# Performance work log

Hardware: AMD Instinct MI355X
Metric: run time of the kernel (lower is better)

The kernel has to match this reference:

```python
import jax, jax.numpy as jnp
import numpy as np

NUM_GROUPS = 32
NUM_HEADS = 8
EPS = 1e-5


def setup_inputs() -> dict:
    key = jax.random.key(0)
    ks = jax.random.split(key, 4)
    b, c, h, w = 16, 512, 32, 32
    x = jax.random.normal(ks[0], (b, c, h, w), dtype=jnp.float32)
    norm_w = jnp.ones((c,), dtype=jnp.float32)
    norm_b = jnp.zeros((c,), dtype=jnp.float32)
    qkv_w = jax.random.normal(ks[1], (3 * c, c), dtype=jnp.float32) * (1.0 / np.sqrt(c))
    qkv_b = jnp.zeros((3 * c,), dtype=jnp.float32)
    proj_w = jax.random.normal(ks[2], (c, c), dtype=jnp.float32) * (1.0 / np.sqrt(c))
    proj_b = jnp.zeros((c,), dtype=jnp.float32)
    return {"x": x, "norm_w": norm_w, "norm_b": norm_b,
            "qkv_w": qkv_w, "qkv_b": qkv_b, "proj_w": proj_w, "proj_b": proj_b}


def group_norm(x, weight, bias):
    b, c, h, w = x.shape
    xg = x.reshape(b, NUM_GROUPS, c // NUM_GROUPS, h * w)
    mean = xg.mean(axis=(2, 3), keepdims=True)
    var = xg.var(axis=(2, 3), keepdims=True)
    xn = (xg - mean) * jax.lax.rsqrt(var + EPS)
    xn = xn.reshape(b, c, h, w)
    return xn * weight[None, :, None, None] + bias[None, :, None, None]


def reference(x, norm_w, norm_b, qkv_w, qkv_b, proj_w, proj_b):
    b, c, h, w = x.shape
    n = h * w
    head = NUM_HEADS
    ch = c // head

    x_norm = group_norm(x, norm_w, norm_b)
    # 1x1 conv == channel matmul: [b,3c,n]
    xf = x_norm.reshape(b, c, n)
    qkv = jnp.einsum('oc,bcn->bon', qkv_w, xf) + qkv_b[None, :, None]
    q, k, v = jnp.split(qkv, 3, axis=1)  # each [b,c,n]
    q = q.reshape(b, head, ch, n) * (ch ** -0.5)
    k = k.reshape(b, head, ch, n)
    v = v.reshape(b, head, ch, n)

    attn = jnp.einsum('bhcn,bhcm->bhnm', q, k)
    attn = jax.nn.softmax(attn, axis=-1)
    out = jnp.einsum('bhnm,bhcm->bhcn', attn, v)  # [b,head,ch,n]
    out = out.reshape(b, c, n)
    out = jnp.einsum('oc,bcn->bon', proj_w, out) + proj_b[None, :, None]
    return x + out.reshape(b, c, h, w)
```

## Files before the change

kernel.cpp:

```cpp
#include <hip/hip_runtime.h>

typedef short short8 __attribute__((ext_vector_type(8)));
typedef float f32x4 __attribute__((ext_vector_type(4)));

#define B_   16
#define C_   512
#define N_   1024
#define NH_  8
#define CH_  64
#define G_   32
#define CPG_ 16

__device__ inline float b2f(unsigned int u) {
    union { unsigned int i; float f; } v; v.i = u << 16; return v.f;
}
__device__ inline unsigned short f2b(float f) {
    union { float f; unsigned int i; } v; v.f = f;
    unsigned int r = v.i + 0x7fffu + ((v.i >> 16) & 1u);
    return (unsigned short)(r >> 16);
}
__device__ inline unsigned int pack2(float a, float b) {
    return (unsigned int)f2b(a) | ((unsigned int)f2b(b) << 16);
}
__device__ inline unsigned int asu(float f) {
    union { float f; unsigned int i; } v; v.f = f; return v.i;
}
__device__ inline unsigned int packtr(float a, float b) {
    return __builtin_amdgcn_perm(asu(b), asu(a), 0x07060302u);
}
__device__ inline void gload16(const void* g, void* l) {
    __builtin_amdgcn_global_load_lds(
        (const __attribute__((address_space(1))) void*)g,
        (__attribute__((address_space(3))) void*)l, 16, 0, 0);
}

__global__ __launch_bounds__(256) void gnconv_kernel(const float* __restrict__ x,
                                                     const float* __restrict__ nw,
                                                     const float* __restrict__ nb,
                                                     unsigned short* __restrict__ xnT,
                                                     const float* __restrict__ qkvw,
                                                     const float* __restrict__ projw,
                                                     unsigned short* __restrict__ wq,
                                                     unsigned short* __restrict__ wp)
{
    __shared__ float red[8];
    __shared__ unsigned short T[64 * 17];
    int t = threadIdx.x;

    if (blockIdx.x >= 512) {
        const int NQ = 3 * C_ * C_;
        int idx = (((int)blockIdx.x - 512) * 256 + t) * 8;
        const float* src; unsigned short* dst; int j;
        if (idx < NQ) { src = qkvw;  dst = wq; j = idx; }
        else          { src = projw; dst = wp; j = idx - NQ; }
        float4 u0 = *(const float4*)(src + j);
        float4 u1 = *(const float4*)(src + j + 4);
        uint4 p;
        p.x = pack2(u0.x, u0.y); p.y = pack2(u0.z, u0.w);
        p.z = pack2(u1.x, u1.y); p.w = pack2(u1.z, u1.w);
        *(uint4*)(dst + j) = p;
        return;
    }

    int b = blockIdx.x >> 5, g = blockIdx.x & 31;
    const float* base = x + ((size_t)(b * C_ + g * CPG_)) * N_;

    float s = 0.f, ss = 0.f;
    for (int it = 0; it < 16; ++it) {
        int idx = (it * 256 + t) * 4;
        float4 u = *(const float4*)(base + idx);
        s  += u.x + u.y + u.z + u.w;
        ss += u.x * u.x + u.y * u.y + u.z * u.z + u.w * u.w;
    }
#pragma unroll
    for (int off = 1; off < 64; off <<= 1) {
        s  += __shfl_xor(s, off);
        ss += __shfl_xor(ss, off);
    }
    int wv = t >> 6;
    if ((t & 63) == 0) { red[wv * 2] = s; red[wv * 2 + 1] = ss; }
    __syncthreads();
    s  = red[0] + red[2] + red[4] + red[6];
    ss = red[1] + red[3] + red[5] + red[7];
    float mean = s * (1.f / 16384.f);
    float var  = ss * (1.f / 16384.f) - mean * mean;
    float rstd = rsqrtf(var + 1e-5f);

    int cl = t >> 4, nn4 = (t & 15) * 4;
    float sc = nw[g * CPG_ + cl] * rstd;
    float sh = nb[g * CPG_ + cl] - mean * sc;
    int nlB = t >> 2, c4 = (t & 3) * 4;

    for (int ch = 0; ch < 16; ++ch) {
        int n0 = ch * 64;
        float4 u = *(const float4*)(base + (size_t)cl * N_ + n0 + nn4);
        T[(nn4 + 0) * 17 + cl] = f2b(u.x * sc + sh);
        T[(nn4 + 1) * 17 + cl] = f2b(u.y * sc + sh);
        T[(nn4 + 2) * 17 + cl] = f2b(u.z * sc + sh);
        T[(nn4 + 3) * 17 + cl] = f2b(u.w * sc + sh);
        __syncthreads();
        ushort4 o;
        o.x = T[nlB * 17 + c4 + 0];
        o.y = T[nlB * 17 + c4 + 1];
        o.z = T[nlB * 17 + c4 + 2];
        o.w = T[nlB * 17 + c4 + 3];
        *(ushort4*)(xnT + ((size_t)(b * N_ + n0 + nlB)) * C_ + g * CPG_ + c4) = o;
        __syncthreads();
    }
}

__global__ __launch_bounds__(256) void qkv_kernel(const unsigned short* __restrict__ w,
                                                  const float* __restrict__ bias,
                                                  const unsigned short* __restrict__ xnT,
                                                  unsigned short* __restrict__ qT,
                                                  unsigned short* __restrict__ kT,
                                                  unsigned short* __restrict__ vv)
{
    __shared__ unsigned short Als[128 * 32], Bls[128 * 32];
    int t = threadIdx.x;
    int n0 = blockIdx.x * 128, m0 = blockIdx.y * 128, b = blockIdx.z;
    int lane = t & 63, wv = t >> 6;
    int l = lane & 15, qd = lane >> 4;
    int wm = (wv >> 1) * 64, wn = (wv & 1) * 64;
    f32x4 acc[4][4] = {};
    const unsigned short* Bbase = xnT + ((size_t)(b * N_ + n0)) * C_;

    int lr = lane >> 2, bpos = lane & 3;
    int r0 = wv * 32 + lr, r1 = r0 + 16;
    int c0 = (bpos ^ ((r0 >> 1) & 3)) * 8;
    int c1 = (bpos ^ ((r1 >> 1) & 3)) * 8;
    const unsigned short* gA0 = w + (size_t)(m0 + r0) * C_ + c0;
    const unsigned short* gA1 = w + (size_t)(m0 + r1) * C_ + c1;
    const unsigned short* gB0 = Bbase + (size_t)r0 * C_ + c0;
    const unsigned short* gB1 = Bbase + (size_t)r1 * C_ + c1;
    unsigned short* lA0 = &Als[(wv * 32) * 32];
    unsigned short* lA1 = &Als[(wv * 32 + 16) * 32];
    unsigned short* lB0 = &Bls[(wv * 32) * 32];
    unsigned short* lB1 = &Bls[(wv * 32 + 16) * 32];

    int aoff[4], boff[4];
#pragma unroll
    for (int i = 0; i < 4; ++i) {
        int ra = wm + i * 16 + l;
        aoff[i] = ra * 32 + ((qd ^ ((ra >> 1) & 3)) * 8);
        int rb = wn + i * 16 + l;
        boff[i] = rb * 32 + ((qd ^ ((rb >> 1) & 3)) * 8);
    }

    for (int kk = 0; kk < 16; ++kk) {
        int ko = kk * 32;
        gload16(gA0 + ko, lA0); gload16(gA1 + ko, lA1);
        gload16(gB0 + ko, lB0); gload16(gB1 + ko, lB1);
        __builtin_amdgcn_s_waitcnt(0);
        __syncthreads();
        short8 aF[4], bF[4];
#pragma unroll
        for (int i = 0; i < 4; ++i) {
            aF[i] = *(const short8*)&Als[aoff[i]];
            bF[i] = *(const short8*)&Bls[boff[i]];
        }
#pragma unroll
        for (int mt = 0; mt < 4; ++mt)
#pragma unroll
            for (int nt = 0; nt < 4; ++nt)
                acc[mt][nt] = __builtin_amdgcn_mfma_f32_16x16x32_bf16(aF[mt], bF[nt], acc[mt][nt], 0, 0, 0);
        __syncthreads();
    }

    int o_base = m0 + wm;
    int sec = o_base >> 9;
    int oc = o_base & 511;
    int h = oc >> 6;
    float bv[4][4];
#pragma unroll
    for (int mt = 0; mt < 4; ++mt)
#pragma unroll
        for (int r = 0; r < 4; ++r)
            bv[mt][r] = bias[o_base + mt * 16 + qd * 4 + r];

    if (sec < 2) {
        unsigned short* dst = (sec == 0) ? qT : kT;
        float scl = (sec == 0) ? (0.125f * 1.44269504f) : 1.0f;
#pragma unroll
        for (int mt = 0; mt < 4; ++mt)
#pragma unroll
            for (int nt = 0; nt < 4; ++nt) {
                int n = n0 + wn + nt * 16 + l;
                ushort4 o;
                o.x = f2b((acc[mt][nt][0] + bv[mt][0]) * scl);
                o.y = f2b((acc[mt][nt][1] + bv[mt][1]) * scl);
                o.z = f2b((acc[mt][nt][2] + bv[mt][2]) * scl);
                o.w = f2b((acc[mt][nt][3] + bv[mt][3]) * scl);
                *(ushort4*)(dst + ((size_t)(b * NH_ + h) * N_ + n) * CH_ + mt * 16 + qd * 4) = o;
            }
    } else {
#pragma unroll
        for (int mt = 0; mt < 4; ++mt)
#pragma unroll
            for (int nt = 0; nt < 4; ++nt) {
                int n = n0 + wn + nt * 16 + l;
#pragma unroll
                for (int r = 0; r < 4; ++r) {
                    int ch = mt * 16 + qd * 4 + r;
                    vv[((size_t)(b * NH_ + h) * CH_ + ch) * N_ + n] = f2b(acc[mt][nt][r] + bv[mt][r]);
                }
            }
    }
}

__global__ __launch_bounds__(256, 4) void attn_kernel(const unsigned short* __restrict__ qT,
                                                      const unsigned short* __restrict__ kT,
                                                      const unsigned short* __restrict__ vv,
                                                      unsigned short* __restrict__ at)
{
    __shared__ unsigned short Ks[2][4096];
    __shared__ unsigned short Vs[2][4096];

    int t = threadIdx.x, lane = t & 63, wv = t >> 6;
    int l = lane & 15, qd = lane >> 4;
    int blk = blockIdx.x;
    int ibk = blk >> 7;
    int bh  = blk & 127;
    int h = bh & 7, b = bh >> 3;
    int i0 = ibk * 128 + wv * 32;
    const size_t hoff = (size_t)bh * (size_t)N_ * CH_;
    const unsigned short* qbase = qT + hoff;
    const unsigned short* kbase = kT + hoff;
    const unsigned short* vbase = vv + hoff;

    int plok;
    {
        unsigned int ta = (unsigned int)lane, tb = 64u + (unsigned int)lane;
        asm volatile("v_permlane32_swap_b32 %0, %1" : "+v"(ta), "+v"(tb));
        asm volatile("v_permlane16_swap_b32 %0, %1" : "+v"(ta), "+v"(tb));
        unsigned int e1 = (unsigned int)((lane >> 4) * 32 + (lane & 15));
        plok = __all(ta == e1) && __all(tb == e1 + 16u);
    }

    short8 qF[2][2];
#pragma unroll
    for (int it = 0; it < 2; ++it)
#pragma unroll
        for (int ks = 0; ks < 2; ++ks)
            qF[it][ks] = *(const short8*)(qbase + (size_t)(i0 + it * 16 + l) * CH_ + ks * 32 + qd * 8);

    int srow = t >> 2, sc16 = (t & 3) * 16;
    int sw = srow & 7, bb = (t & 3) * 2;
    int d0 = srow * 64 + ((bb ^ sw) * 8);
    int d1 = srow * 64 + (((bb + 1) ^ sw) * 8);
    const unsigned short* kSrc = kbase + (size_t)srow * CH_ + sc16;
    const unsigned short* vSrc = vbase + (size_t)srow * N_ + sc16;

    f32x4 Oa[4][2] = {};
    float lsum[2] = {0.f, 0.f};
    int la0 = (qd & 1) * 32 + l;
    int la1 = la0 + 16;
    int swl = l & 7;

    uint4 ku0, ku1, vu0, vu1;
    {
        const uint4* kp = (const uint4*)(kSrc);
        ku0 = kp[0]; ku1 = kp[1];
        const uint4* vp2 = (const uint4*)(vSrc);
        vu0 = vp2[0]; vu1 = vp2[1];
        *(uint4*)&Ks[0][d0] = ku0; *(uint4*)&Ks[0][d1] = ku1;
        *(uint4*)&Vs[0][d0] = vu0; *(uint4*)&Vs[0][d1] = vu1;
        kp  = (const uint4*)(kSrc + 4096);
        ku0 = kp[0]; ku1 = kp[1];
        vp2 = (const uint4*)(vSrc + 64);
        vu0 = vp2[0]; vu1 = vp2[1];
    }

    for (int tile = 0; tile < 16; ++tile) {
        __syncthreads();
        if (tile < 15) {
            unsigned short* Kw = Ks[(tile + 1) & 1];
            unsigned short* Vw = Vs[(tile + 1) & 1];
            *(uint4*)&Kw[d0] = ku0; *(uint4*)&Kw[d1] = ku1;
            *(uint4*)&Vw[d0] = vu0; *(uint4*)&Vw[d1] = vu1;
            if (tile < 14) {
                const uint4* kp = (const uint4*)(kSrc + (size_t)(tile + 2) * 4096);
                ku0 = kp[0]; ku1 = kp[1];
                const uint4* vp2 = (const uint4*)(vSrc + (size_t)(tile + 2) * 64);
                vu0 = vp2[0]; vu1 = vp2[1];
            }
        }
        const unsigned short* Kb = Ks[tile & 1];
        const unsigned short* Vb = Vs[tile & 1];
#pragma unroll
        for (int jb = 0; jb < 2; ++jb) {
            short8 kA[2][2];
#pragma unroll
            for (int jt = 0; jt < 2; ++jt)
#pragma unroll
                for (int ks = 0; ks < 2; ++ks)
                    kA[jt][ks] = *(const short8*)&Kb[(jb * 32 + jt * 16 + l) * 64 + (((ks * 4 + qd) ^ swl) * 8)];
            f32x4 Sa[2][2] = {};
#pragma unroll
            for (int jt = 0; jt < 2; ++jt)
#pragma unroll
                for (int it = 0; it < 2; ++it)
#pragma unroll
                    for (int ks = 0; ks < 2; ++ks)
                        Sa[jt][it] = __builtin_amdgcn_mfma_f32_16x16x32_bf16(kA[jt][ks], qF[it][ks], Sa[jt][it], 0, 0, 0);
            unsigned int pk[2][2][2];
#pragma unroll
            for (int jt = 0; jt < 2; ++jt)
#pragma unroll
                for (int it = 0; it < 2; ++it) {
                    float p0 = __builtin_amdgcn_exp2f(Sa[jt][it][0]);
                    float p1 = __builtin_amdgcn_exp2f(Sa[jt][it][1]);
                    float p2 = __builtin_amdgcn_exp2f(Sa[jt][it][2]);
                    float p3 = __builtin_amdgcn_exp2f(Sa[jt][it][3]);
                    lsum[it] += (p0 + p1) + (p2 + p3);
                    pk[jt][it][0] = packtr(p0, p1);
                    pk[jt][it][1] = packtr(p2, p3);
                }
            short8 bP[2];
            if (plok) {
#pragma unroll
                for (int it = 0; it < 2; ++it) {
                    union { short8 s; unsigned int u[4]; } fb;
                    unsigned int a0 = pk[0][it][0], c0 = pk[1][it][0];
                    asm volatile("v_permlane32_swap_b32 %0, %1" : "+v"(a0), "+v"(c0));
                    asm volatile("v_permlane16_swap_b32 %0, %1" : "+v"(a0), "+v"(c0));
                    unsigned int a1 = pk[0][it][1], c1 = pk[1][it][1];
                    asm volatile("v_permlane32_swap_b32 %0, %1" : "+v"(a1), "+v"(c1));
                    asm volatile("v_permlane16_swap_b32 %0, %1" : "+v"(a1), "+v"(c1));
                    fb.u[0] = a0; fb.u[1] = a1; fb.u[2] = c0; fb.u[3] = c1;
                    bP[it] = fb.s;
                }
            } else {
#pragma unroll
                for (int it = 0; it < 2; ++it) {
                    union { short8 s; unsigned int u[4]; } fb;
                    unsigned int a0 = (unsigned int)__shfl((int)pk[0][it][0], la0);
                    unsigned int b0 = (unsigned int)__shfl((int)pk[1][it][0], la0);
                    fb.u[0] = (qd < 2) ? a0 : b0;
                    unsigned int a1 = (unsigned int)__shfl((int)pk[0][it][1], la0);
                    unsigned int b1 = (unsigned int)__shfl((int)pk[1][it][1], la0);
                    fb.u[1] = (qd < 2) ? a1 : b1;
                    unsigned int a2 = (unsigned int)__shfl((int)pk[0][it][0], la1);
                    unsigned int b2 = (unsigned int)__shfl((int)pk[1][it][0], la1);
                    fb.u[2] = (qd < 2) ? a2 : b2;
                    unsigned int a3 = (unsigned int)__shfl((int)pk[0][it][1], la1);
                    unsigned int b3 = (unsigned int)__shfl((int)pk[1][it][1], la1);
                    fb.u[3] = (qd < 2) ? a3 : b3;
                    bP[it] = fb.s;
                }
            }
            short8 vA[4];
#pragma unroll
            for (int cht = 0; cht < 4; ++cht)
                vA[cht] = *(const short8*)&Vb[(cht * 16 + l) * 64 + (((jb * 4 + qd) ^ swl) * 8)];
#pragma unroll
            for (int cht = 0; cht < 4; ++cht)
#pragma unroll
                for (int it = 0; it < 2; ++it)
                    Oa[cht][it] = __builtin_amdgcn_mfma_f32_16x16x32_bf16(vA[cht], bP[it], Oa[cht][it], 0, 0, 0);
        }
    }

#pragma unroll
    for (int it = 0; it < 2; ++it) {
        float lt = lsum[it];
        lt += __shfl_xor(lt, 16);
        lt += __shfl_xor(lt, 32);
        float inv = 1.0f / lt;
        int i = i0 + it * 16 + l;
        unsigned short* dst = at + ((size_t)(b * N_ + i)) * C_ + h * CH_;
#pragma unroll
        for (int cht = 0; cht < 4; ++cht) {
            ushort4 o;
            o.x = f2b(Oa[cht][it][0] * inv);
            o.y = f2b(Oa[cht][it][1] * inv);
            o.z = f2b(Oa[cht][it][2] * inv);
            o.w = f2b(Oa[cht][it][3] * inv);
            *(ushort4*)(dst + cht * 16 + qd * 4) = o;
        }
    }
}

__global__ __launch_bounds__(256) void proj_kernel(const unsigned short* __restrict__ w,
                                                   const float* __restrict__ bias,
                                                   const unsigned short* __restrict__ at,
                                                   const float* __restrict__ x,
                                                   float* __restrict__ out)
{
    __shared__ unsigned short Als[128 * 32], Bls[128 * 32];
    int t = threadIdx.x;
    int n0 = blockIdx.x * 128, m0 = blockIdx.y * 128, b = blockIdx.z;
    int lane = t & 63, wv = t >> 6;
    int l = lane & 15, qd = lane >> 4;
    int wm = (wv >> 1) * 64, wn = (wv & 1) * 64;
    f32x4 acc[4][4] = {};
    const unsigned short* Bbase = at + ((size_t)(b * N_ + n0)) * C_;

    int lr = lane >> 2, bpos = lane & 3;
    int r0 = wv * 32 + lr, r1 = r0 + 16;
    int c0 = (bpos ^ ((r0 >> 1) & 3)) * 8;
    int c1 = (bpos ^ ((r1 >> 1) & 3)) * 8;
    const unsigned short* gA0 = w + (size_t)(m0 + r0) * C_ + c0;
    const unsigned short* gA1 = w + (size_t)(m0 + r1) * C_ + c1;
    const unsigned short* gB0 = Bbase + (size_t)r0 * C_ + c0;
    const unsigned short* gB1 = Bbase + (size_t)r1 * C_ + c1;
    unsigned short* lA0 = &Als[(wv * 32) * 32];
    unsigned short* lA1 = &Als[(wv * 32 + 16) * 32];
    unsigned short* lB0 = &Bls[(wv * 32) * 32];
    unsigned short* lB1 = &Bls[(wv * 32 + 16) * 32];

    int aoff[4], boff[4];
#pragma unroll
    for (int i = 0; i < 4; ++i) {
        int ra = wm + i * 16 + l;
        aoff[i] = ra * 32 + ((qd ^ ((ra >> 1) & 3)) * 8);
        int rb = wn + i * 16 + l;
        boff[i] = rb * 32 + ((qd ^ ((rb >> 1) & 3)) * 8);
    }

    for (int kk = 0; kk < 16; ++kk) {
        int ko = kk * 32;
        gload16(gA0 + ko, lA0); gload16(gA1 + ko, lA1);
        gload16(gB0 + ko, lB0); gload16(gB1 + ko, lB1);
        __builtin_amdgcn_s_waitcnt(0);
        __syncthreads();
        short8 aF[4], bF[4];
#pragma unroll
        for (int i = 0; i < 4; ++i) {
            aF[i] = *(const short8*)&Als[aoff[i]];
            bF[i] = *(const short8*)&Bls[boff[i]];
        }
#pragma unroll
        for (int mt = 0; mt < 4; ++mt)
#pragma unroll
            for (int nt = 0; nt < 4; ++nt)
                acc[mt][nt] = __builtin_amdgcn_mfma_f32_16x16x32_bf16(aF[mt], bF[nt], acc[mt][nt], 0, 0, 0);
        __syncthreads();
    }

    float bv[4][4];
#pragma unroll
    for (int mt = 0; mt < 4; ++mt)
#pragma unroll
        for (int r = 0; r < 4; ++r)
            bv[mt][r] = bias[m0 + wm + mt * 16 + qd * 4 + r];

#pragma unroll
    for (int mt = 0; mt < 4; ++mt)
#pragma unroll
        for (int nt = 0; nt < 4; ++nt) {
            int n = n0 + wn + nt * 16 + l;
#pragma unroll
            for (int r = 0; r < 4; ++r) {
                int o = m0 + wm + mt * 16 + qd * 4 + r;
                size_t idx = ((size_t)b * C_ + o) * N_ + n;
                out[idx] = acc[mt][nt][r] + bv[mt][r] + x[idx];
            }
        }
}

extern "C" void kernel_launch(void* const* d_in, const int* in_sizes, int n_in,
                              void* d_out, int out_size, void* d_ws, size_t ws_size,
                              hipStream_t stream) {
    const float* x     = (const float*)d_in[0];
    const float* nw    = (const float*)d_in[1];
    const float* nb    = (const float*)d_in[2];
    const float* qkvw  = (const float*)d_in[3];
    const float* qkvb  = (const float*)d_in[4];
    const float* projw = (const float*)d_in[5];
    const float* projb = (const float*)d_in[6];
    float* out = (float*)d_out;
    char* ws = (char*)d_ws;
    const size_t SZ = (size_t)B_ * N_ * C_ * 2;
    unsigned short* xnT = (unsigned short*)(ws);
    unsigned short* qTp = (unsigned short*)(ws + SZ);
    unsigned short* kTp = (unsigned short*)(ws + 2 * SZ);
    unsigned short* vp  = (unsigned short*)(ws + 3 * SZ);
    unsigned short* atp = (unsigned short*)(ws);
    unsigned short* wq  = (unsigned short*)(ws + 4 * SZ);
    unsigned short* wp  = (unsigned short*)(ws + 4 * SZ + (size_t)3 * C_ * C_ * 2);

    hipLaunchKernelGGL(gnconv_kernel, dim3(1024), dim3(256), 0, stream, x, nw, nb, xnT, qkvw, projw, wq, wp);
    hipLaunchKernelGGL(qkv_kernel,    dim3(8, 12, B_), dim3(256), 0, stream, wq, qkvb, xnT, qTp, kTp, vp);
    hipLaunchKernelGGL(attn_kernel,   dim3(1024), dim3(256), 0, stream, qTp, kTp, vp, atp);
    hipLaunchKernelGGL(proj_kernel,   dim3(8, 4, B_), dim3(256), 0, stream, wp, projb, atp, x, out);
}
```

Before: 219.1 us.

## Widen GEMM K-tile to 64, drop LDS transpose in groupnorm, batch attention tile

The QKV and projection GEMMs now stage a 64-wide K slice per iteration with an 8-way XOR swizzle, which halves the loop trips and barrier pairs. The cost is double the LDS per block. The groupnorm kernel no longer transposes through shared memory with two barriers per chunk. Each thread instead loads all 16 channels for two positions and writes 32-byte bf16 rows directly. The attention inner loop is restructured to issue both key sub-blocks' loads, QK MFMAs, exps and P permutes together before the PV MFMAs, giving more ILP at the cost of more registers.

```diff
diff --git a/kernel.cpp b/kernel.cpp
--- a/kernel.cpp
+++ b/kernel.cpp
@@ -44,7 +44,6 @@
                                                      unsigned short* __restrict__ wp)
 {
     __shared__ float red[8];
-    __shared__ unsigned short T[64 * 17];
     int t = threadIdx.x;
 
     if (blockIdx.x >= 512) {
@@ -86,26 +85,39 @@
     float var  = ss * (1.f / 16384.f) - mean * mean;
     float rstd = rsqrtf(var + 1e-5f);
 
-    int cl = t >> 4, nn4 = (t & 15) * 4;
-    float sc = nw[g * CPG_ + cl] * rstd;
-    float sh = nb[g * CPG_ + cl] - mean * sc;
-    int nlB = t >> 2, c4 = (t & 3) * 4;
-
+    float sc[16], sh[16];
+#pragma unroll
     for (int ch = 0; ch < 16; ++ch) {
-        int n0 = ch * 64;
-        float4 u = *(const float4*)(base + (size_t)cl * N_ + n0 + nn4);
-        T[(nn4 + 0) * 17 + cl] = f2b(u.x * sc + sh);
-        T[(nn4 + 1) * 17 + cl] = f2b(u.y * sc + sh);
-        T[(nn4 + 2) * 17 + cl] = f2b(u.z * sc + sh);
-        T[(nn4 + 3) * 17 + cl] = f2b(u.w * sc + sh);
-        __syncthreads();
-        ushort4 o;
-        o.x = T[nlB * 17 + c4 + 0];
-        o.y = T[nlB * 17 + c4 + 1];
-        o.z = T[nlB * 17 + c4 + 2];
-        o.w = T[nlB * 17 + c4 + 3];
-        *(ushort4*)(xnT + ((size_t)(b * N_ + n0 + nlB)) * C_ + g * CPG_ + c4) = o;
-        __syncthreads();
+        float wv_ = nw[g * CPG_ + ch];
+        float bv_ = nb[g * CPG_ + ch];
+        sc[ch] = wv_ * rstd;
+        sh[ch] = bv_ - mean * sc[ch];
+    }
+
+#pragma unroll
+    for (int nbi = 0; nbi < 2; ++nbi) {
+        int n = nbi * 512 + t * 2;
+        float2 v[16];
+#pragma unroll
+        for (int ch = 0; ch < 16; ++ch)
+            v[ch] = *(const float2*)(base + (size_t)ch * N_ + n);
+#pragma unroll
+        for (int col = 0; col < 2; ++col) {
+            float f[16];
+#pragma unroll
+            for (int ch = 0; ch < 16; ++ch) {
+                float xv = col ? v[ch].y : v[ch].x;
+                f[ch] = xv * sc[ch] + sh[ch];
+            }
+            uint4 o0, o1;
+            o0.x = pack2(f[0], f[1]);  o0.y = pack2(f[2], f[3]);
+            o0.z = pack2(f[4], f[5]);  o0.w = pack2(f[6], f[7]);
+            o1.x = pack2(f[8], f[9]);  o1.y = pack2(f[10], f[11]);
+            o1.z = pack2(f[12], f[13]); o1.w = pack2(f[14], f[15]);
+            unsigned short* dst = xnT + ((size_t)(b * N_ + n + col)) * C_ + g * CPG_;
+            *(uint4*)dst = o0;
+            *(uint4*)(dst + 8) = o1;
+        }
     }
 }
 
@@ -116,7 +128,7 @@
                                                   unsigned short* __restrict__ kT,
                                                   unsigned short* __restrict__ vv)
 {
-    __shared__ unsigned short Als[128 * 32], Bls[128 * 32];
+    __shared__ unsigned short Als[128 * 64], Bls[128 * 64];
     int t = threadIdx.x;
     int n0 = blockIdx.x * 128, m0 = blockIdx.y * 128, b = blockIdx.z;
     int lane = t & 63, wv = t >> 6;
@@ -125,45 +137,43 @@
     f32x4 acc[4][4] = {};
     const unsigned short* Bbase = xnT + ((size_t)(b * N_ + n0)) * C_;
 
-    int lr = lane >> 2, bpos = lane & 3;
-    int r0 = wv * 32 + lr, r1 = r0 + 16;
-    int c0 = (bpos ^ ((r0 >> 1) & 3)) * 8;
-    int c1 = (bpos ^ ((r1 >> 1) & 3)) * 8;
-    const unsigned short* gA0 = w + (size_t)(m0 + r0) * C_ + c0;
-    const unsigned short* gA1 = w + (size_t)(m0 + r1) * C_ + c1;
-    const unsigned short* gB0 = Bbase + (size_t)r0 * C_ + c0;
-    const unsigned short* gB1 = Bbase + (size_t)r1 * C_ + c1;
-    unsigned short* lA0 = &Als[(wv * 32) * 32];
-    unsigned short* lA1 = &Als[(wv * 32 + 16) * 32];
-    unsigned short* lB0 = &Bls[(wv * 32) * 32];
-    unsigned short* lB1 = &Bls[(wv * 32 + 16) * 32];
-
-    int aoff[4], boff[4];
-#pragma unroll
-    for (int i = 0; i < 4; ++i) {
-        int ra = wm + i * 16 + l;
-        aoff[i] = ra * 32 + ((qd ^ ((ra >> 1) & 3)) * 8);
-        int rb = wn + i * 16 + l;
-        boff[i] = rb * 32 + ((qd ^ ((rb >> 1) & 3)) * 8);
-    }
-
-    for (int kk = 0; kk < 16; ++kk) {
-        int ko = kk * 32;
-        gload16(gA0 + ko, lA0); gload16(gA1 + ko, lA1);
-        gload16(gB0 + ko, lB0); gload16(gB1 + ko, lB1);
+    int grow = lane >> 3, gcol = ((lane & 7) ^ grow) * 8;
+    const unsigned short* pA[4]; const unsigned short* pB[4];
+    unsigned short* lA[4]; unsigned short* lB[4];
+#pragma unroll
+    for (int g = 0; g < 4; ++g) {
+        int r = wv * 32 + g * 8 + grow;
+        pA[g] = w + (size_t)(m0 + r) * C_ + gcol;
+        pB[g] = Bbase + (size_t)r * C_ + gcol;
+        lA[g] = &Als[(wv * 32 + g * 8) * 64];
+        lB[g] = &Bls[(wv * 32 + g * 8) * 64];
+    }
+
+    for (int kk = 0; kk < 8; ++kk) {
+        int ko = kk * 64;
+#pragma unroll
+        for (int g = 0; g < 4; ++g) {
+            gload16(pA[g] + ko, lA[g]);
+            gload16(pB[g] + ko, lB[g]);
+        }
         __builtin_amdgcn_s_waitcnt(0);
         __syncthreads();
-        short8 aF[4], bF[4];
-#pragma unroll
-        for (int i = 0; i < 4; ++i) {
-            aF[i] = *(const short8*)&Als[aoff[i]];
-            bF[i] = *(const short8*)&Bls[boff[i]];
-        }
-#pragma unroll
-        for (int mt = 0; mt < 4; ++mt)
-#pragma unroll
-            for (int nt = 0; nt < 4; ++nt)
-                acc[mt][nt] = __builtin_amdgcn_mfma_f32_16x16x32_bf16(aF[mt], bF[nt], acc[mt][nt], 0, 0, 0);
+#pragma unroll
+        for (int ks = 0; ks < 2; ++ks) {
+            short8 aF[4], bF[4];
+#pragma unroll
+            for (int i = 0; i < 4; ++i) {
+                int ra = wm + i * 16 + l;
+                aF[i] = *(const short8*)&Als[ra * 64 + (((ks * 4 + qd) ^ (l & 7)) * 8)];
+                int rb = wn + i * 16 + l;
+                bF[i] = *(const short8*)&Bls[rb * 64 + (((ks * 4 + qd) ^ (l & 7)) * 8)];
+            }
+#pragma unroll
+            for (int mt = 0; mt < 4; ++mt)
+#pragma unroll
+                for (int nt = 0; nt < 4; ++nt)
+                    acc[mt][nt] = __builtin_amdgcn_mfma_f32_16x16x32_bf16(aF[mt], bF[nt], acc[mt][nt], 0, 0, 0);
+        }
         __syncthreads();
     }
 
@@ -287,68 +297,85 @@
         }
         const unsigned short* Kb = Ks[tile & 1];
         const unsigned short* Vb = Vs[tile & 1];
-#pragma unroll
-        for (int jb = 0; jb < 2; ++jb) {
-            short8 kA[2][2];
+
+        short8 kA[2][2][2];
+#pragma unroll
+        for (int jb = 0; jb < 2; ++jb)
 #pragma unroll
             for (int jt = 0; jt < 2; ++jt)
 #pragma unroll
                 for (int ks = 0; ks < 2; ++ks)
-                    kA[jt][ks] = *(const short8*)&Kb[(jb * 32 + jt * 16 + l) * 64 + (((ks * 4 + qd) ^ swl) * 8)];
-            f32x4 Sa[2][2] = {};
+                    kA[jb][jt][ks] = *(const short8*)&Kb[(jb * 32 + jt * 16 + l) * 64 + (((ks * 4 + qd) ^ swl) * 8)];
+        f32x4 Sa[2][2][2] = {};
+#pragma unroll
+        for (int jb = 0; jb < 2; ++jb)
 #pragma unroll
             for (int jt = 0; jt < 2; ++jt)
 #pragma unroll
                 for (int it = 0; it < 2; ++it)
 #pragma unroll
                     for (int ks = 0; ks < 2; ++ks)
-                        Sa[jt][it] = __builtin_amdgcn_mfma_f32_16x16x32_bf16(kA[jt][ks], qF[it][ks], Sa[jt][it], 0, 0, 0);
-            unsigned int pk[2][2][2];
+                        Sa[jb][jt][it] = __builtin_amdgcn_mfma_f32_16x16x32_bf16(kA[jb][jt][ks], qF[it][ks], Sa[jb][jt][it], 0, 0, 0);
+
+        unsigned int pk[2][2][2][2];
+        float ls0 = 0.f, ls1 = 0.f;
+#pragma unroll
+        for (int jb = 0; jb < 2; ++jb)
 #pragma unroll
             for (int jt = 0; jt < 2; ++jt)
 #pragma unroll
                 for (int it = 0; it < 2; ++it) {
-                    float p0 = __builtin_amdgcn_exp2f(Sa[jt][it][0]);
-                    float p1 = __builtin_amdgcn_exp2f(Sa[jt][it][1]);
-                    float p2 = __builtin_amdgcn_exp2f(Sa[jt][it][2]);
-                    float p3 = __builtin_amdgcn_exp2f(Sa[jt][it][3]);
-                    lsum[it] += (p0 + p1) + (p2 + p3);
-                    pk[jt][it][0] = packtr(p0, p1);
-                    pk[jt][it][1] = packtr(p2, p3);
+                    float p0 = __builtin_amdgcn_exp2f(Sa[jb][jt][it][0]);
+                    float p1 = __builtin_amdgcn_exp2f(Sa[jb][jt][it][1]);
+                    float p2 = __builtin_amdgcn_exp2f(Sa[jb][jt][it][2]);
+                    float p3 = __builtin_amdgcn_exp2f(Sa[jb][jt][it][3]);
+                    float q01 = (p0 + p1) + (p2 + p3);
+                    if (it == 0) ls0 += q01; else ls1 += q01;
+                    pk[jb][jt][it][0] = packtr(p0, p1);
+                    pk[jb][jt][it][1] = packtr(p2, p3);
                 }
-            short8 bP[2];
-            if (plok) {
+        lsum[0] += ls0; lsum[1] += ls1;
+
+        short8 bP[2][2];
+        if (plok) {
+#pragma unroll
+            for (int jb = 0; jb < 2; ++jb)
 #pragma unroll
                 for (int it = 0; it < 2; ++it) {
                     union { short8 s; unsigned int u[4]; } fb;
-                    unsigned int a0 = pk[0][it][0], c0 = pk[1][it][0];
+                    unsigned int a0 = pk[jb][0][it][0], c0 = pk[jb][1][it][0];
                     asm volatile("v_permlane32_swap_b32 %0, %1" : "+v"(a0), "+v"(c0));
                     asm volatile("v_permlane16_swap_b32 %0, %1" : "+v"(a0), "+v"(c0));
-                    unsigned int a1 = pk[0][it][1], c1 = pk[1][it][1];
+                    unsigned int a1 = pk[jb][0][it][1], c1 = pk[jb][1][it][1];
                     asm volatile("v_permlane32_swap_b32 %0, %1" : "+v"(a1), "+v"(c1));
                     asm volatile("v_permlane16_swap_b32 %0, %1" : "+v"(a1), "+v"(c1));
                     fb.u[0] = a0; fb.u[1] = a1; fb.u[2] = c0; fb.u[3] = c1;
-                    bP[it] = fb.s;
+                    bP[jb][it] = fb.s;
                 }
-            } else {
+        } else {
+#pragma unroll
+            for (int jb = 0; jb < 2; ++jb)
 #pragma unroll
                 for (int it = 0; it < 2; ++it) {
                     union { short8 s; unsigned int u[4]; } fb;
-                    unsigned int a0 = (unsigned int)__shfl((int)pk[0][it][0], la0);
-                    unsigned int b0 = (unsigned int)__shfl((int)pk[1][it][0], la0);
+                    unsigned int a0 = (unsigned int)__shfl((int)pk[jb][0][it][0], la0);
+                    unsigned int b0 = (unsigned int)__shfl((int)pk[jb][1][it][0], la0);
                     fb.u[0] = (qd < 2) ? a0 : b0;
-                    unsigned int a1 = (unsigned int)__shfl((int)pk[0][it][1], la0);
-                    unsigned int b1 = (unsigned int)__shfl((int)pk[1][it][1], la0);
+                    unsigned int a1 = (unsigned int)__shfl((int)pk[jb][0][it][1], la0);
+                    unsigned int b1 = (unsigned int)__shfl((int)pk[jb][1][it][1], la0);
                     fb.u[1] = (qd < 2) ? a1 : b1;
-                    unsigned int a2 = (unsigned int)__shfl((int)pk[0][it][0], la1);
-                    unsigned int b2 = (unsigned int)__shfl((int)pk[1][it][0], la1);
+                    unsigned int a2 = (unsigned int)__shfl((int)pk[jb][0][it][0], la1);
+                    unsigned int b2 = (unsigned int)__shfl((int)pk[jb][1][it][0], la1);
                     fb.u[2] = (qd < 2) ? a2 : b2;
-                    unsigned int a3 = (unsigned int)__shfl((int)pk[0][it][1], la1);
-                    unsigned int b3 = (unsigned int)__shfl((int)pk[1][it][1], la1);
+                    unsigned int a3 = (unsigned int)__shfl((int)pk[jb][0][it][1], la1);
+                    unsigned int b3 = (unsigned int)__shfl((int)pk[jb][1][it][1], la1);
                     fb.u[3] = (qd < 2) ? a3 : b3;
-                    bP[it] = fb.s;
+                    bP[jb][it] = fb.s;
                 }
-            }
+        }
+
+#pragma unroll
+        for (int jb = 0; jb < 2; ++jb) {
             short8 vA[4];
 #pragma unroll
             for (int cht = 0; cht < 4; ++cht)
@@ -357,7 +384,7 @@
             for (int cht = 0; cht < 4; ++cht)
 #pragma unroll
                 for (int it = 0; it < 2; ++it)
-                    Oa[cht][it] = __builtin_amdgcn_mfma_f32_16x16x32_bf16(vA[cht], bP[it], Oa[cht][it], 0, 0, 0);
+                    Oa[cht][it] = __builtin_amdgcn_mfma_f32_16x16x32_bf16(vA[cht], bP[jb][it], Oa[cht][it], 0, 0, 0);
         }
     }
 
@@ -387,7 +414,7 @@
                                                    const float* __restrict__ x,
                                                    float* __restrict__ out)
 {
-    __shared__ unsigned short Als[128 * 32], Bls[128 * 32];
+    __shared__ unsigned short Als[128 * 64], Bls[128 * 64];
     int t = threadIdx.x;
     int n0 = blockIdx.x * 128, m0 = blockIdx.y * 128, b = blockIdx.z;
     int lane = t & 63, wv = t >> 6;
@@ -396,45 +423,43 @@
     f32x4 acc[4][4] = {};
     const unsigned short* Bbase = at + ((size_t)(b * N_ + n0)) * C_;
 
-    int lr = lane >> 2, bpos = lane & 3;
-    int r0 = wv * 32 + lr, r1 = r0 + 16;
-    int c0 = (bpos ^ ((r0 >> 1) & 3)) * 8;
-    int c1 = (bpos ^ ((r1 >> 1) & 3)) * 8;
-    const unsigned short* gA0 = w + (size_t)(m0 + r0) * C_ + c0;
-    const unsigned short* gA1 = w + (size_t)(m0 + r1) * C_ + c1;
-    const unsigned short* gB0 = Bbase + (size_t)r0 * C_ + c0;
-    const unsigned short* gB1 = Bbase + (size_t)r1 * C_ + c1;
-    unsigned short* lA0 = &Als[(wv * 32) * 32];
-    unsigned short* lA1 = &Als[(wv * 32 + 16) * 32];
-    unsigned short* lB0 = &Bls[(wv * 32) * 32];
-    unsigned short* lB1 = &Bls[(wv * 32 + 16) * 32];
-
-    int aoff[4], boff[4];
-#pragma unroll
-    for (int i = 0; i < 4; ++i) {
-        int ra = wm + i * 16 + l;
-        aoff[i] = ra * 32 + ((qd ^ ((ra >> 1) & 3)) * 8);
-        int rb = wn + i * 16 + l;
-        boff[i] = rb * 32 + ((qd ^ ((rb >> 1) & 3)) * 8);
-    }
-
-    for (int kk = 0; kk < 16; ++kk) {
-        int ko = kk * 32;
-        gload16(gA0 + ko, lA0); gload16(gA1 + ko, lA1);
-        gload16(gB0 + ko, lB0); gload16(gB1 + ko, lB1);
+    int grow = lane >> 3, gcol = ((lane & 7) ^ grow) * 8;
+    const unsigned short* pA[4]; const unsigned short* pB[4];
+    unsigned short* lA[4]; unsigned short* lB[4];
+#pragma unroll
+    for (int g = 0; g < 4; ++g) {
+        int r = wv * 32 + g * 8 + grow;
+        pA[g] = w + (size_t)(m0 + r) * C_ + gcol;
+        pB[g] = Bbase + (size_t)r * C_ + gcol;
+        lA[g] = &Als[(wv * 32 + g * 8) * 64];
+        lB[g] = &Bls[(wv * 32 + g * 8) * 64];
+    }
+
+    for (int kk = 0; kk < 8; ++kk) {
+        int ko = kk * 64;
+#pragma unroll
+        for (int g = 0; g < 4; ++g) {
+            gload16(pA[g] + ko, lA[g]);
+            gload16(pB[g] + ko, lB[g]);
+        }
         __builtin_amdgcn_s_waitcnt(0);
         __syncthreads();
-        short8 aF[4], bF[4];
-#pragma unroll
-        for (int i = 0; i < 4; ++i) {
-            aF[i] = *(const short8*)&Als[aoff[i]];
-            bF[i] = *(const short8*)&Bls[boff[i]];
-        }
-#pragma unroll
-        for (int mt = 0; mt < 4; ++mt)
-#pragma unroll
-            for (int nt = 0; nt < 4; ++nt)
-                acc[mt][nt] = __builtin_amdgcn_mfma_f32_16x16x32_bf16(aF[mt], bF[nt], acc[mt][nt], 0, 0, 0);
+#pragma unroll
+        for (int ks = 0; ks < 2; ++ks) {
+            short8 aF[4], bF[4];
+#pragma unroll
+            for (int i = 0; i < 4; ++i) {
+                int ra = wm + i * 16 + l;
+                aF[i] = *(const short8*)&Als[ra * 64 + (((ks * 4 + qd) ^ (l & 7)) * 8)];
+                int rb = wn + i * 16 + l;
+                bF[i] = *(const short8*)&Bls[rb * 64 + (((ks * 4 + qd) ^ (l & 7)) * 8)];
+            }
+#pragma unroll
+            for (int mt = 0; mt < 4; ++mt)
+#pragma unroll
+                for (int nt = 0; nt < 4; ++nt)
+                    acc[mt][nt] = __builtin_amdgcn_mfma_f32_16x16x32_bf16(aF[mt], bF[nt], acc[mt][nt], 0, 0, 0);
+        }
         __syncthreads();
     }
 
```

After: 233.6 us. +6.7%, slower.
